# Kernel optimization log

Hardware: AMD Instinct MI355X
Metric: run time of the kernel (lower is better)

The kernel has to match this reference:

```python
import jax, jax.numpy as jnp
import numpy as np

D = 1024
H = 16
HD = D // H  # per-head dim = 64
LQ = 2048
LK = 2048


def setup_inputs() -> dict:
    key = jax.random.key(0)
    ks = jax.random.split(key, 6)
    scale = 1.0 / np.sqrt(D)
    return {
        "input_embeddings": jax.random.normal(ks[0], (LQ, D), dtype=jnp.float32),
        "history_hidden": jax.random.normal(ks[1], (LK, D), dtype=jnp.float32),
        "W_q": jax.random.normal(ks[2], (D, D), dtype=jnp.float32) * scale,
        "W_k": jax.random.normal(ks[3], (D, D), dtype=jnp.float32) * scale,
        "W_v": jax.random.normal(ks[4], (D, D), dtype=jnp.float32) * scale,
        "W_o": jax.random.normal(ks[5], (D, D), dtype=jnp.float32) * scale,
    }


def reference(input_embeddings, history_hidden, W_q, W_k, W_v, W_o):
    # nn.Linear(bias=False): y = x @ W.T ; weights are [out, in]
    q = (input_embeddings @ W_q.T).reshape(LQ, H, HD)  # [Lq, H, hd]
    k = (history_hidden @ W_k.T).reshape(LK, H, HD)    # [Lk, H, hd]
    v = (history_hidden @ W_v.T).reshape(LK, H, HD)    # [Lk, H, hd]
    # per-head scaled dot-product attention, batched over heads
    scores = jnp.einsum("qhd,khd->hqk", q, k) / np.sqrt(HD).astype(np.float32)
    attn = jax.nn.softmax(scores, axis=-1)             # [H, Lq, Lk]
    ctx = jnp.einsum("hqk,khd->qhd", attn, v).reshape(LQ, D)
    # dropout p=0.0 -> identity
    return ctx @ W_o.T
```

## Files before the change

### kernel.cpp

```cpp
#include <hip/hip_runtime.h>

typedef __bf16 bf16x8 __attribute__((ext_vector_type(8)));
typedef __bf16 bf16x4 __attribute__((ext_vector_type(4)));
typedef float f32x4 __attribute__((ext_vector_type(4)));
typedef float f32x16 __attribute__((ext_vector_type(16)));
typedef unsigned short u16x4 __attribute__((ext_vector_type(4)));
typedef unsigned short u16x8 __attribute__((ext_vector_type(8)));

#define LQS 2048
#define LKS 2048
#define DMODEL 1024
#define NH 16
#define HDIM 64
#define NSPLIT 4

#if __has_builtin(__builtin_amdgcn_exp2f)
#define EXP2(x) __builtin_amdgcn_exp2f(x)
#else
#define EXP2(x) exp2f(x)
#endif

__device__ __forceinline__ unsigned short f2bf(float f) {
  union { float f; unsigned int u; } v; v.f = f;
  unsigned int r = v.u + 0x7FFFu + ((v.u >> 16) & 1u);
  return (unsigned short)(r >> 16);
}

__device__ __forceinline__ unsigned int pk2(float a, float b) {
  __bf16 lo = (__bf16)a, hi = (__bf16)b;
  unsigned short ul = __builtin_bit_cast(unsigned short, lo);
  unsigned short uh = __builtin_bit_cast(unsigned short, hi);
  return (unsigned)ul | ((unsigned)uh << 16);
}

#define ASYNC_CP16(gp, lp)                                                     \
  __builtin_amdgcn_global_load_lds(                                            \
      (const __attribute__((address_space(1))) unsigned int*)(gp),             \
      (__attribute__((address_space(3))) unsigned int*)(lp), 16, 0, 0)

struct CvtDesc { const float* src; unsigned short* dst; float scl; unsigned int nchunk; };
struct CvtBatch { CvtDesc d[6]; };

__global__ __launch_bounds__(256)
void cvt_all_k(CvtBatch cb) {
  unsigned int c = blockIdx.x * 256 + threadIdx.x;
#pragma unroll
  for (int s = 0; s < 6; ++s) {
    if (c < cb.d[s].nchunk) {
      const float* src = cb.d[s].src + (size_t)c * 8;
      float4 a = *(const float4*)(src);
      float4 b = *(const float4*)(src + 4);
      const float scl = cb.d[s].scl;
      u16x8 r;
      r[0] = f2bf(a.x * scl); r[1] = f2bf(a.y * scl);
      r[2] = f2bf(a.z * scl); r[3] = f2bf(a.w * scl);
      r[4] = f2bf(b.x * scl); r[5] = f2bf(b.y * scl);
      r[6] = f2bf(b.z * scl); r[7] = f2bf(b.w * scl);
      *(u16x8*)(cb.d[s].dst + (size_t)c * 8) = r;
      return;
    }
    c -= cb.d[s].nchunk;
  }
}

struct GemmDesc { const unsigned short* A; const unsigned short* B; void* C; int ldc; int transC; };
struct GemmBatch3 { GemmDesc d[3]; };

template<int BM, int BN, bool F32OUT>
__global__ __launch_bounds__(256)
void gemm_bt(GemmBatch3 gb, int K) {
  constexpr int MFR = BM / 32;
  constexpr int NFR = BN / 32;
  const GemmDesc g = gb.d[blockIdx.z];
  __shared__ __align__(16) unsigned short sA[2][BM * 32];
  __shared__ __align__(16) unsigned short sB[2][BN * 32];
  const int tid = threadIdx.x;
  const int w = tid >> 6, l = tid & 63;
  const int wr = w >> 1, wc = w & 1;
  const int lr = l & 15, lk = (l >> 4) * 8;
  const unsigned short* Ab = g.A + (size_t)(blockIdx.y * BM) * K;
  const unsigned short* Bb = g.B + (size_t)(blockIdx.x * BN) * K;
  const int srow = w * 16 + (l >> 2);
  const int scol = (l & 3) * 8;

  auto stage = [&](int buf, int k0) {
#pragma unroll
    for (int ia = 0; ia < BM / 64; ++ia)
      ASYNC_CP16(Ab + (size_t)(ia * 64 + srow) * K + k0 + scol,
                 sA[buf] + ia * 2048 + w * 512);
#pragma unroll
    for (int ib = 0; ib < BN / 64; ++ib)
      ASYNC_CP16(Bb + (size_t)(ib * 64 + srow) * K + k0 + scol,
                 sB[buf] + ib * 2048 + w * 512);
  };

  f32x4 acc[MFR][NFR] = {};
  stage(0, 0);
  __syncthreads();
  int cur = 0;
  for (int k0 = 0; k0 < K; k0 += 32) {
    if (k0 + 32 < K) stage(cur ^ 1, k0 + 32);
    bf16x8 af[MFR], bfr[NFR];
#pragma unroll
    for (int m = 0; m < MFR; ++m)
      af[m] = *(const bf16x8*)(sA[cur] + (wr * (BM / 2) + m * 16 + lr) * 32 + lk);
#pragma unroll
    for (int n = 0; n < NFR; ++n)
      bfr[n] = *(const bf16x8*)(sB[cur] + (wc * (BN / 2) + n * 16 + lr) * 32 + lk);
#pragma unroll
    for (int m = 0; m < MFR; ++m)
#pragma unroll
      for (int n = 0; n < NFR; ++n)
        acc[m][n] = __builtin_amdgcn_mfma_f32_16x16x32_bf16(af[m], bfr[n], acc[m][n], 0, 0, 0);
    __syncthreads();
    cur ^= 1;
  }
  const int r0 = blockIdx.y * BM + wr * (BM / 2) + (l >> 4) * 4;
  const int c0 = blockIdx.x * BN + wc * (BN / 2) + lr;
  if (g.transC) {
#pragma unroll
    for (int m = 0; m < MFR; ++m)
#pragma unroll
      for (int n = 0; n < NFR; ++n) {
        u16x4 v;
#pragma unroll
        for (int r = 0; r < 4; ++r) v[r] = f2bf(acc[m][n][r]);
        *(u16x4*)((unsigned short*)g.C + (size_t)(c0 + n * 16) * g.ldc + r0 + m * 16) = v;
      }
  } else {
#pragma unroll
    for (int m = 0; m < MFR; ++m)
#pragma unroll
      for (int n = 0; n < NFR; ++n)
#pragma unroll
        for (int r = 0; r < 4; ++r) {
          size_t idx = (size_t)(r0 + m * 16 + r) * g.ldc + c0 + n * 16;
          if (F32OUT) ((float*)g.C)[idx] = acc[m][n][r];
          else        ((unsigned short*)g.C)[idx] = f2bf(acc[m][n][r]);
        }
  }
}

__global__ __launch_bounds__(256)
void attn_k(const unsigned short* __restrict__ Q, const unsigned short* __restrict__ K,
            const unsigned short* __restrict__ Vt,
            __bf16* __restrict__ pacc, float* __restrict__ plsum) {
  __shared__ __align__(16) __bf16 sK[2][64 * 64];
  __shared__ __align__(16) __bf16 sV[2][64 * 64];
  const int qt = blockIdx.x, h = blockIdx.y, z = blockIdx.z;
  const int tid = threadIdx.x;
  const int w = tid >> 6, l = tid & 63;
  const int lq = l & 31;
  const int hi = l >> 5;
  const int qw0 = qt * 128 + w * 32;

  const int srow = l >> 3;
  const int scolb = (l & 7) * 16;

  bf16x8 qf[4];
#pragma unroll
  for (int t = 0; t < 4; ++t)
    qf[t] = *(const bf16x8*)(Q + (size_t)(qw0 + lq) * DMODEL + h * HDIM + t * 16 + hi * 8);

  f32x16 accO[2] = {};
  float lrun = 0.f;

  const int kt0 = z * (LKS / NSPLIT), kt1 = kt0 + LKS / NSPLIT;

#define STAGE(B, KT)                                                           \
  do {                                                                         \
    _Pragma("unroll")                                                          \
    for (int i_ = 0; i_ < 2; ++i_) {                                           \
      const int row_ = (w * 2 + i_) * 8 + srow;                                \
      const int sc_ = scolb ^ ((row_ & 7) << 4);                               \
      ASYNC_CP16(K + (size_t)((KT) + row_) * DMODEL + h * HDIM + sc_ / 2,      \
                 (char*)(&sK[B][0]) + (w * 2 + i_) * 1024);                    \
      ASYNC_CP16(Vt + (size_t)(h * HDIM + row_) * LKS + (KT) + sc_ / 2,        \
                 (char*)(&sV[B][0]) + (w * 2 + i_) * 1024);                    \
    }                                                                          \
  } while (0)

  STAGE(0, kt0);
  __syncthreads();
  int cur = 0;

  for (int kt = kt0; kt < kt1; kt += 64) {
    if (kt + 64 < kt1) STAGE(cur ^ 1, kt + 64);

    f32x16 sc[2] = {};
#pragma unroll
    for (int kb = 0; kb < 2; ++kb)
#pragma unroll
      for (int t = 0; t < 4; ++t) {
        const int krow = kb * 32 + lq;
        const int cb = (t * 32 + hi * 16) ^ ((krow & 7) << 4);
        bf16x8 kf = *(const bf16x8*)((const char*)(&sK[cur][0]) + krow * 128 + cb);
        sc[kb] = __builtin_amdgcn_mfma_f32_32x32x16_bf16(kf, qf[t], sc[kb], 0, 0, 0);
      }
#pragma unroll
    for (int kb = 0; kb < 2; ++kb)
#pragma unroll
      for (int r = 0; r < 16; ++r) {
        float p = EXP2(sc[kb][r]);
        sc[kb][r] = p;
        lrun += p;
      }
    unsigned int wd[2][8];
#pragma unroll
    for (int kb = 0; kb < 2; ++kb)
#pragma unroll
      for (int g = 0; g < 8; ++g)
        wd[kb][g] = pk2(sc[kb][2 * g], sc[kb][2 * g + 1]);

#if __has_builtin(__builtin_amdgcn_mfma_f32_32x32x8bf16_1k)
    union W2 { unsigned int u[2]; bf16x4 v; };
#pragma unroll
    for (int g = 0; g < 8; ++g) {
      W2 a;
      a.u[0] = wd[g >> 2][2 * (g & 3)];
      a.u[1] = wd[g >> 2][2 * (g & 3) + 1];
#pragma unroll
      for (int db = 0; db < 2; ++db) {
        const int vrow = db * 32 + lq;
        const int cb = (16 * g + 8 * hi) ^ ((vrow & 7) << 4);
        bf16x4 bv = *(const bf16x4*)((const char*)(&sV[cur][0]) + vrow * 128 + cb);
        accO[db] = __builtin_amdgcn_mfma_f32_32x32x8bf16_1k(a.v, bv, accO[db], 0, 0, 0);
      }
    }
#else
    union PA { unsigned int u[4]; bf16x8 v; };
    PA pa[4];
#pragma unroll
    for (int ks = 0; ks < 4; ++ks) {
      const int kb = ks >> 1;
      const int g0 = (ks & 1) * 4;
      const unsigned int own0 = wd[kb][g0],     own1 = wd[kb][g0 + 1];
      const unsigned int oth0 = wd[kb][g0 + 2], oth1 = wd[kb][g0 + 3];
      const unsigned int off0 = hi ? own0 : oth0;
      const unsigned int off1 = hi ? own1 : oth1;
      const unsigned int rcv0 = (unsigned int)__shfl_xor((int)off0, 32);
      const unsigned int rcv1 = (unsigned int)__shfl_xor((int)off1, 32);
      pa[ks].u[0] = hi ? rcv0 : own0;
      pa[ks].u[1] = hi ? rcv1 : own1;
      pa[ks].u[2] = hi ? oth0 : rcv0;
      pa[ks].u[3] = hi ? oth1 : rcv1;
    }
#pragma unroll
    for (int db = 0; db < 2; ++db)
#pragma unroll
      for (int ks = 0; ks < 4; ++ks) {
        const int vrow = db * 32 + lq;
        const int cb = (ks * 32 + hi * 16) ^ ((vrow & 7) << 4);
        bf16x8 vf = *(const bf16x8*)((const char*)(&sV[cur][0]) + vrow * 128 + cb);
        accO[db] = __builtin_amdgcn_mfma_f32_32x32x16_bf16(pa[ks].v, vf, accO[db], 0, 0, 0);
      }
#endif
    __syncthreads();
    cur ^= 1;
  }
#undef STAGE

  lrun += __shfl_xor(lrun, 32);
  if (hi == 0)
    plsum[((size_t)z * NH + h) * LQS + qw0 + lq] = lrun;
#pragma unroll
  for (int db = 0; db < 2; ++db)
#pragma unroll
    for (int r = 0; r < 16; ++r) {
      const int q = qw0 + (r & 3) + 8 * (r >> 2) + 4 * hi;
      pacc[(size_t)z * LQS * DMODEL + (size_t)q * DMODEL + h * HDIM + db * 32 + lq] =
          (__bf16)accO[db][r];
    }
}

__global__ __launch_bounds__(256)
void combine_k(const __bf16* pacc, const float* __restrict__ plsum, __bf16* ctx) {
  const size_t e = ((size_t)blockIdx.x * 256 + threadIdx.x) * 8;
  const int row = (int)(e >> 10), d0 = (int)(e & 1023), h = d0 >> 6;
  float lsum = 0.f;
  float acc[8] = {};
#pragma unroll
  for (int z = 0; z < NSPLIT; ++z) {
    lsum += plsum[((size_t)z * NH + h) * LQS + row];
    bf16x8 v = *(const bf16x8*)(pacc + (size_t)z * LQS * DMODEL + e);
#pragma unroll
    for (int j = 0; j < 8; ++j) acc[j] += (float)v[j];
  }
  float inv = 1.0f / lsum;
  bf16x8 r;
#pragma unroll
  for (int j = 0; j < 8; ++j) r[j] = (__bf16)(acc[j] * inv);
  *(bf16x8*)(ctx + e) = r;
}

extern "C" void kernel_launch(void* const* d_in, const int* in_sizes, int n_in,
                              void* d_out, int out_size, void* d_ws, size_t ws_size,
                              hipStream_t stream) {
  const float* x  = (const float*)d_in[0];
  const float* hh = (const float*)d_in[1];
  const float* wq = (const float*)d_in[2];
  const float* wk = (const float*)d_in[3];
  const float* wv = (const float*)d_in[4];
  const float* wo = (const float*)d_in[5];

  unsigned short* ws = (unsigned short*)d_ws;
  const size_t E2 = (size_t)LQS * DMODEL;
  const size_t E1 = (size_t)DMODEL * DMODEL;
  const size_t M = 1048576;
  unsigned short* xb  = ws;
  unsigned short* hb  = ws + 2 * M;
  unsigned short* wqb = ws + 4 * M;
  unsigned short* wkb = ws + 5 * M;
  unsigned short* wvb = ws + 6 * M;
  unsigned short* wob = ws + 8 * M;
  unsigned short* Qb  = ws + 9 * M;
  unsigned short* Kb  = ws + 11 * M;
  unsigned short* Vtb = ws + 13 * M;
  __bf16* pacc  = (__bf16*)ws;
  float*  plsum = (float*)(ws + 15 * M);
  unsigned short* cxb = ws;
  const float SCL = 0.125f * 1.4426950408889634f;

  CvtBatch cb;
  cb.d[0] = { x,  xb,  SCL, (unsigned)(E2 / 8) };
  cb.d[1] = { hh, hb,  1.f, (unsigned)(E2 / 8) };
  cb.d[2] = { wq, wqb, 1.f, (unsigned)(E1 / 8) };
  cb.d[3] = { wk, wkb, 1.f, (unsigned)(E1 / 8) };
  cb.d[4] = { wv, wvb, 1.f, (unsigned)(E1 / 8) };
  cb.d[5] = { wo, wob, 1.f, (unsigned)(E1 / 8) };
  cvt_all_k<<<dim3(4096), 256, 0, stream>>>(cb);

  GemmBatch3 qkv;
  qkv.d[0] = { xb, wqb, (void*)Qb,  DMODEL, 0 };
  qkv.d[1] = { hb, wkb, (void*)Kb,  DMODEL, 0 };
  qkv.d[2] = { hb, wvb, (void*)Vtb, LKS,    1 };
  gemm_bt<64, 128, false><<<dim3(DMODEL / 128, LQS / 64, 3), 256, 0, stream>>>(qkv, DMODEL);

  attn_k<<<dim3(LQS / 128, NH, NSPLIT), 256, 0, stream>>>(Qb, Kb, Vtb, pacc, plsum);

  combine_k<<<dim3((unsigned)(E2 / 2048)), 256, 0, stream>>>(pacc, plsum, (__bf16*)cxb);

  GemmBatch3 fin = {};
  fin.d[0] = { cxb, wob, d_out, DMODEL, 0 };
  gemm_bt<64, 64, true><<<dim3(DMODEL / 64, LQS / 64, 1), 256, 0, stream>>>(fin, DMODEL);
}
```

Before: 92.29 us.

## Triple-buffer K/V staging with vmcnt waits and MFMA-based row sums

Replaces the double-buffered K/V LDS pipeline with a fully unrolled three-stage ring that keeps two tiles in flight. It uses explicit s_waitcnt vmcnt counts and raw s_barrier instead of __syncthreads. It also computes the softmax denominator with an extra MFMA against a ones vector, replacing 32 scalar adds per tile. LDS use grows by half, which may lower occupancy, and the row sum is now taken from bf16-rounded probabilities.

```diff
diff --git a/kernel.cpp b/kernel.cpp
--- a/kernel.cpp
+++ b/kernel.cpp
@@ -13,11 +13,18 @@
 #define NH 16
 #define HDIM 64
 #define NSPLIT 4
+#define NT 8
 
 #if __has_builtin(__builtin_amdgcn_exp2f)
 #define EXP2(x) __builtin_amdgcn_exp2f(x)
 #else
 #define EXP2(x) exp2f(x)
+#endif
+
+#if __has_builtin(__builtin_amdgcn_mfma_f32_32x32x8bf16_1k)
+#define HAS_K8 1
+#else
+#define HAS_K8 0
 #endif
 
 __device__ __forceinline__ unsigned short f2bf(float f) {
@@ -145,8 +152,8 @@
 void attn_k(const unsigned short* __restrict__ Q, const unsigned short* __restrict__ K,
             const unsigned short* __restrict__ Vt,
             __bf16* __restrict__ pacc, float* __restrict__ plsum) {
-  __shared__ __align__(16) __bf16 sK[2][64 * 64];
-  __shared__ __align__(16) __bf16 sV[2][64 * 64];
+  __shared__ __align__(16) __bf16 sK[3][64 * 64];
+  __shared__ __align__(16) __bf16 sV[3][64 * 64];
   const int qt = blockIdx.x, h = blockIdx.y, z = blockIdx.z;
   const int tid = threadIdx.x;
   const int w = tid >> 6, l = tid & 63;
@@ -163,9 +170,16 @@
     qf[t] = *(const bf16x8*)(Q + (size_t)(qw0 + lq) * DMODEL + h * HDIM + t * 16 + hi * 8);
 
   f32x16 accO[2] = {};
+#if HAS_K8
+  f32x16 accsum = {};
+  bf16x4 onesv;
+#pragma unroll
+  for (int j = 0; j < 4; ++j) onesv[j] = (__bf16)1.0f;
+#else
   float lrun = 0.f;
-
-  const int kt0 = z * (LKS / NSPLIT), kt1 = kt0 + LKS / NSPLIT;
+#endif
+
+  const int kt0 = z * (LKS / NSPLIT);
 
 #define STAGE(B, KT)                                                           \
   do {                                                                         \
@@ -181,30 +195,37 @@
   } while (0)
 
   STAGE(0, kt0);
-  __syncthreads();
-  int cur = 0;
-
-  for (int kt = kt0; kt < kt1; kt += 64) {
-    if (kt + 64 < kt1) STAGE(cur ^ 1, kt + 64);
+  STAGE(1, kt0 + 64);
+
+#pragma unroll
+  for (int t = 0; t < NT; ++t) {
+    if (t >= 1) {
+      __builtin_amdgcn_sched_barrier(0);
+      __builtin_amdgcn_s_barrier();
+    }
+    if (t + 2 < NT) STAGE((t + 2) % 3, kt0 + (t + 2) * 64);
+    if (t < NT - 2)       asm volatile("s_waitcnt vmcnt(8)" ::: "memory");
+    else if (t == NT - 2) asm volatile("s_waitcnt vmcnt(4)" ::: "memory");
+    else                  asm volatile("s_waitcnt vmcnt(0)" ::: "memory");
+    __builtin_amdgcn_s_barrier();
+    __builtin_amdgcn_sched_barrier(0);
+    const int cur = t % 3;
 
     f32x16 sc[2] = {};
 #pragma unroll
     for (int kb = 0; kb < 2; ++kb)
 #pragma unroll
-      for (int t = 0; t < 4; ++t) {
+      for (int tt = 0; tt < 4; ++tt) {
         const int krow = kb * 32 + lq;
-        const int cb = (t * 32 + hi * 16) ^ ((krow & 7) << 4);
+        const int cb = (tt * 32 + hi * 16) ^ ((krow & 7) << 4);
         bf16x8 kf = *(const bf16x8*)((const char*)(&sK[cur][0]) + krow * 128 + cb);
-        sc[kb] = __builtin_amdgcn_mfma_f32_32x32x16_bf16(kf, qf[t], sc[kb], 0, 0, 0);
+        sc[kb] = __builtin_amdgcn_mfma_f32_32x32x16_bf16(kf, qf[tt], sc[kb], 0, 0, 0);
       }
 #pragma unroll
     for (int kb = 0; kb < 2; ++kb)
 #pragma unroll
-      for (int r = 0; r < 16; ++r) {
-        float p = EXP2(sc[kb][r]);
-        sc[kb][r] = p;
-        lrun += p;
-      }
+      for (int r = 0; r < 16; ++r)
+        sc[kb][r] = EXP2(sc[kb][r]);
     unsigned int wd[2][8];
 #pragma unroll
     for (int kb = 0; kb < 2; ++kb)
@@ -212,7 +233,7 @@
       for (int g = 0; g < 8; ++g)
         wd[kb][g] = pk2(sc[kb][2 * g], sc[kb][2 * g + 1]);
 
-#if __has_builtin(__builtin_amdgcn_mfma_f32_32x32x8bf16_1k)
+#if HAS_K8
     union W2 { unsigned int u[2]; bf16x4 v; };
 #pragma unroll
     for (int g = 0; g < 8; ++g) {
@@ -226,8 +247,13 @@
         bf16x4 bv = *(const bf16x4*)((const char*)(&sV[cur][0]) + vrow * 128 + cb);
         accO[db] = __builtin_amdgcn_mfma_f32_32x32x8bf16_1k(a.v, bv, accO[db], 0, 0, 0);
       }
-    }
-#else
+      accsum = __builtin_amdgcn_mfma_f32_32x32x8bf16_1k(a.v, onesv, accsum, 0, 0, 0);
+    }
+#else
+#pragma unroll
+    for (int kb = 0; kb < 2; ++kb)
+#pragma unroll
+      for (int r = 0; r < 16; ++r) lrun += sc[kb][r];
     union PA { unsigned int u[4]; bf16x8 v; };
     PA pa[4];
 #pragma unroll
@@ -255,14 +281,20 @@
         accO[db] = __builtin_amdgcn_mfma_f32_32x32x16_bf16(pa[ks].v, vf, accO[db], 0, 0, 0);
       }
 #endif
-    __syncthreads();
-    cur ^= 1;
   }
 #undef STAGE
 
+#if HAS_K8
+  if (lq == 0) {
+#pragma unroll
+    for (int r = 0; r < 16; ++r)
+      plsum[((size_t)z * NH + h) * LQS + qw0 + (r & 3) + 8 * (r >> 2) + 4 * hi] = accsum[r];
+  }
+#else
   lrun += __shfl_xor(lrun, 32);
   if (hi == 0)
     plsum[((size_t)z * NH + h) * LQS + qw0 + lq] = lrun;
+#endif
 #pragma unroll
   for (int db = 0; db < 2; ++db)
 #pragma unroll
```

New measurement: 92.03 us. Within noise of the previous version (-0.3%).
